# Kernel optimization log

Hardware: AMD Instinct MI355X
Metric: run time of the kernel (lower is better)

## Reference

```python
import jax, jax.numpy as jnp
import numpy as np

N_USERS = 200000
N_ITEMS = 50000
F = 64          # n_factors
B = 32768       # batch of (user, item) pairs
L = 256         # ratings per user (dense-ified ragged lists)
MIN_R = 1
MAX_R = 5


def setup_inputs() -> dict:
    key = jax.random.key(0)
    ks = jax.random.split(key, 8)
    # xavier_normal_ std = sqrt(2 / (fan_in + fan_out))
    std_u = (2.0 / (N_USERS + F)) ** 0.5
    std_i = (2.0 / (N_ITEMS + F)) ** 0.5
    user_factors = jax.random.normal(ks[0], (N_USERS, F), dtype=jnp.float32) * std_u
    item_factors = jax.random.normal(ks[1], (N_ITEMS, F), dtype=jnp.float32) * std_i
    user_biases = jax.random.normal(ks[2], (N_USERS, 1), dtype=jnp.float32)
    item_biases = jax.random.normal(ks[3], (N_ITEMS, 1), dtype=jnp.float32)
    # integer star ratings in [MIN_R, MAX_R], one dense row per user
    ratings = jax.random.randint(ks[4], (N_USERS, L), MIN_R, MAX_R + 1).astype(jnp.float32)
    users = jax.random.randint(ks[5], (B,), 0, N_USERS)
    items = jax.random.randint(ks[6], (B,), 0, N_ITEMS)
    item_pos = jax.random.randint(ks[7], (B,), 0, L)  # position of the item in the user's rating row
    return {
        "users": users, "items": items, "item_pos": item_pos,
        "ratings": ratings,
        "user_factors": user_factors, "item_factors": item_factors,
        "user_biases": user_biases, "item_biases": item_biases,
        "min_rating": MIN_R, "max_rating": MAX_R,
    }


def reference(users, items, item_pos, ratings, user_factors, item_factors,
              user_biases, item_biases, min_rating, max_rating):
    b = users.shape[0]
    # MF prediction: biases + dot(user_factor, item_factor), shape [B, 1]
    pred = (user_biases[users] + item_biases[items]
            + jnp.sum(user_factors[users] * item_factors[items], axis=1, keepdims=True))
    p = pred[:, 0]  # [B]

    # per-sample: user's rating row with this item's rating replaced by the prediction
    rows = ratings[users]                                   # [B, L]
    rows = rows.at[jnp.arange(b), item_pos].set(p)          # batched index-update

    # torch.histc(bins=max_rating, min=min_rating, max=max_rating):
    # width = (max - min) / bins; values outside [min, max] ignored; x == max -> last bin
    bins = max_rating
    width = (max_rating - min_rating) / bins
    idx = jnp.floor((rows - min_rating) / width)
    idx = jnp.where(rows == max_rating, bins - 1, idx)      # [B, L]
    in_range = (rows >= min_rating) & (rows <= max_rating)

    # end bin from rounded prediction: clip(round(p), max(min-1, 0), max-1)
    end = jnp.clip(jnp.round(p), max(min_rating - 1, 0), max_rating - 1)  # [B]

    # mass = sum(hist[0:end+1]) - 0.5 * hist[end]  == count(idx<=end) - 0.5*count(idx==end)
    le = jnp.where(in_range & (idx <= end[:, None]), 1.0, 0.0)
    eq = jnp.where(in_range & (idx == end[:, None]), 1.0, 0.0)
    mass = jnp.sum(le - 0.5 * eq, axis=1, keepdims=True)    # [B, 1]

    return jnp.stack((pred, mass), axis=1)                   # [B, 2, 1]
```

## Files before the change

### kernel.cpp

```cpp
#include <hip/hip_runtime.h>

constexpr int EPW = 8;

__global__ __launch_bounds__(256) void hist_mf_kernel(
    const int*   __restrict__ users,
    const int*   __restrict__ items,
    const int*   __restrict__ item_pos,
    const float* __restrict__ ratings,
    const float* __restrict__ user_factors,
    const float* __restrict__ item_factors,
    const float* __restrict__ user_biases,
    const float* __restrict__ item_biases,
    const int*   __restrict__ minr_p,
    const int*   __restrict__ maxr_p,
    int L, int F, int B,
    float* __restrict__ out)
{
    const int wv   = threadIdx.x >> 6;
    const int lane = threadIdx.x & 63;
    const int wave = blockIdx.x * (blockDim.x >> 6) + wv;
    const int e0   = wave * EPW;
    if (e0 >= B) return;

    const int minr = *minr_p, maxr = *maxr_p;
    const int bins = maxr;
    const float fmin  = (float)minr;
    const float fmax  = (float)maxr;
    const float width = (float)(maxr - minr) / (float)bins;
    const float invw  = 1.0f / width;
    const float lo    = (float)((minr - 1) > 0 ? minr - 1 : 0);
    const float hi    = (float)(maxr - 1);

    int u[EPW], it[EPW], ps[EPW];
    #pragma unroll
    for (int k = 0; k < EPW; ++k) {
        int e = min(e0 + k, B - 1);
        u[k]  = users[e];
        it[k] = items[e];
        ps[k] = item_pos[e];
    }

    const float* rowp[EPW];
    #pragma unroll
    for (int k = 0; k < EPW; ++k) rowp[k] = ratings + (size_t)u[k] * L;

    const int nchunk = ((L & 3) == 0) ? (L >> 8) : 0;
    float4 r4[EPW];
    #pragma unroll
    for (int k = 0; k < EPW; ++k)
        r4[k] = (nchunk > 0) ? reinterpret_cast<const float4*>(rowp[k])[lane]
                             : make_float4(0.f, 0.f, 0.f, 0.f);

    float d[EPW];
    #pragma unroll
    for (int k = 0; k < EPW; ++k) d[k] = 0.f;
    for (int f = lane; f < F; f += 64) {
        #pragma unroll
        for (int k = 0; k < EPW; ++k)
            d[k] += user_factors[(size_t)u[k] * F + f] *
                    item_factors[(size_t)it[k] * F + f];
    }
    #pragma unroll
    for (int o = 32; o > 0; o >>= 1) {
        #pragma unroll
        for (int k = 0; k < EPW; ++k) d[k] += __shfl_xor(d[k], o, 64);
    }

    float pred[EPW], endv[EPW], mass[EPW];
    #pragma unroll
    for (int k = 0; k < EPW; ++k) {
        pred[k] = user_biases[u[k]] + item_biases[it[k]] + d[k];
        endv[k] = fminf(fmaxf(rintf(pred[k]), lo), hi);
        mass[k] = 0.f;
    }

    auto accum = [&](float rraw, int j, int pos, float predv, float ev, float& m) {
        float v = (j == pos) ? predv : rraw;
        bool in = (v >= fmin) && (v <= fmax);
        float fidx = floorf((v - fmin) * invw);
        if (v == fmax) fidx = (float)(bins - 1);
        if (in) {
            if (fidx <= ev) m += 1.0f;
            if (fidx == ev) m -= 0.5f;
        }
    };

    if (nchunk > 0) {
        const int j0 = lane * 4;
        #pragma unroll
        for (int k = 0; k < EPW; ++k) {
            accum(r4[k].x, j0 + 0, ps[k], pred[k], endv[k], mass[k]);
            accum(r4[k].y, j0 + 1, ps[k], pred[k], endv[k], mass[k]);
            accum(r4[k].z, j0 + 2, ps[k], pred[k], endv[k], mass[k]);
            accum(r4[k].w, j0 + 3, ps[k], pred[k], endv[k], mass[k]);
        }
    }
    for (int c = 1; c < nchunk; ++c) {
        const int j0 = c * 256 + lane * 4;
        #pragma unroll
        for (int k = 0; k < EPW; ++k) {
            float4 q = reinterpret_cast<const float4*>(rowp[k] + c * 256)[lane];
            accum(q.x, j0 + 0, ps[k], pred[k], endv[k], mass[k]);
            accum(q.y, j0 + 1, ps[k], pred[k], endv[k], mass[k]);
            accum(q.z, j0 + 2, ps[k], pred[k], endv[k], mass[k]);
            accum(q.w, j0 + 3, ps[k], pred[k], endv[k], mass[k]);
        }
    }
    for (int j = (nchunk << 8) + lane; j < L; j += 64) {
        #pragma unroll
        for (int k = 0; k < EPW; ++k)
            accum(rowp[k][j], j, ps[k], pred[k], endv[k], mass[k]);
    }

    #pragma unroll
    for (int o = 32; o > 0; o >>= 1) {
        #pragma unroll
        for (int k = 0; k < EPW; ++k) mass[k] += __shfl_xor(mass[k], o, 64);
    }

    if (lane == 0) {
        const int nv = min(EPW, B - e0);
        if (nv == EPW) {
            #pragma unroll
            for (int q = 0; q < EPW / 2; ++q)
                reinterpret_cast<float4*>(out)[wave * (EPW / 2) + q] =
                    make_float4(pred[2 * q], mass[2 * q],
                                pred[2 * q + 1], mass[2 * q + 1]);
        } else {
            for (int k = 0; k < nv; ++k) {
                out[2 * (e0 + k) + 0] = pred[k];
                out[2 * (e0 + k) + 1] = mass[k];
            }
        }
    }
}

extern "C" void kernel_launch(void* const* d_in, const int* in_sizes, int n_in,
                              void* d_out, int out_size, void* d_ws, size_t ws_size,
                              hipStream_t stream) {
    const int*   users        = (const int*)  d_in[0];
    const int*   items        = (const int*)  d_in[1];
    const int*   item_pos     = (const int*)  d_in[2];
    const float* ratings      = (const float*)d_in[3];
    const float* user_factors = (const float*)d_in[4];
    const float* item_factors = (const float*)d_in[5];
    const float* user_biases  = (const float*)d_in[6];
    const float* item_biases  = (const float*)d_in[7];
    const int*   minr_p       = (const int*)  d_in[8];
    const int*   maxr_p       = (const int*)  d_in[9];

    const int B       = in_sizes[0];
    const int N_USERS = in_sizes[6];
    const int L       = in_sizes[3] / N_USERS;
    const int F       = in_sizes[4] / N_USERS;

    float* out = (float*)d_out;

    const int elemsPerBlock = (256 / 64) * EPW;
    const int grid = (B + elemsPerBlock - 1) / elemsPerBlock;

    hist_mf_kernel<<<grid, 256, 0, stream>>>(
        users, items, item_pos, ratings, user_factors, item_factors,
        user_biases, item_biases, minr_p, maxr_p, L, F, B, out);
}
```

Baseline: 21.16 us.

## Stage rating rows into LDS via global_load_lds and halve elements per wave

Loads each user's rating row directly from global memory into LDS with the asynchronous global_load_lds builtin, in place of register float4 loads. The kernel then waits on vmcnt and reads the row back from LDS for the histogram step. Elements per wave drop from 8 to 4, which doubles the grid and cuts register pressure, aiming for more memory-level parallelism. The cost is 16KB of LDS per block, which may limit occupancy, plus an extra LDS round trip. The direct-to-LDS path only covers L==256; other lengths use a scalar loop.

```diff
diff --git a/kernel.cpp b/kernel.cpp
--- a/kernel.cpp
+++ b/kernel.cpp
@@ -1,6 +1,10 @@
 #include <hip/hip_runtime.h>
 
-constexpr int EPW = 8;
+constexpr int EPW = 4;
+constexpr int WPB = 4;
+
+typedef const __attribute__((address_space(1))) void GAS;
+typedef __attribute__((address_space(3))) void LAS;
 
 __global__ __launch_bounds__(256) void hist_mf_kernel(
     const int*   __restrict__ users,
@@ -16,9 +20,11 @@
     int L, int F, int B,
     float* __restrict__ out)
 {
+    __shared__ __align__(16) float lds[WPB][EPW][256];
+
     const int wv   = threadIdx.x >> 6;
     const int lane = threadIdx.x & 63;
-    const int wave = blockIdx.x * (blockDim.x >> 6) + wv;
+    const int wave = blockIdx.x * WPB + wv;
     const int e0   = wave * EPW;
     if (e0 >= B) return;
 
@@ -44,12 +50,16 @@
     #pragma unroll
     for (int k = 0; k < EPW; ++k) rowp[k] = ratings + (size_t)u[k] * L;
 
-    const int nchunk = ((L & 3) == 0) ? (L >> 8) : 0;
-    float4 r4[EPW];
-    #pragma unroll
-    for (int k = 0; k < EPW; ++k)
-        r4[k] = (nchunk > 0) ? reinterpret_cast<const float4*>(rowp[k])[lane]
-                             : make_float4(0.f, 0.f, 0.f, 0.f);
+    const bool dma = (L == 256);
+    if (dma) {
+        #pragma unroll
+        for (int k = 0; k < EPW; ++k) {
+            __builtin_amdgcn_global_load_lds(
+                (GAS*)(rowp[k] + lane * 4),
+                (LAS*)&lds[wv][k][lane * 4],
+                16, 0, 0);
+        }
+    }
 
     float d[EPW];
     #pragma unroll
@@ -85,31 +95,24 @@
         }
     };
 
-    if (nchunk > 0) {
+    if (dma) {
+        asm volatile("s_waitcnt vmcnt(0)" ::: "memory");
+        __builtin_amdgcn_sched_barrier(0);
         const int j0 = lane * 4;
         #pragma unroll
         for (int k = 0; k < EPW; ++k) {
-            accum(r4[k].x, j0 + 0, ps[k], pred[k], endv[k], mass[k]);
-            accum(r4[k].y, j0 + 1, ps[k], pred[k], endv[k], mass[k]);
-            accum(r4[k].z, j0 + 2, ps[k], pred[k], endv[k], mass[k]);
-            accum(r4[k].w, j0 + 3, ps[k], pred[k], endv[k], mass[k]);
-        }
-    }
-    for (int c = 1; c < nchunk; ++c) {
-        const int j0 = c * 256 + lane * 4;
-        #pragma unroll
-        for (int k = 0; k < EPW; ++k) {
-            float4 q = reinterpret_cast<const float4*>(rowp[k] + c * 256)[lane];
+            float4 q = *reinterpret_cast<const float4*>(&lds[wv][k][lane * 4]);
             accum(q.x, j0 + 0, ps[k], pred[k], endv[k], mass[k]);
             accum(q.y, j0 + 1, ps[k], pred[k], endv[k], mass[k]);
             accum(q.z, j0 + 2, ps[k], pred[k], endv[k], mass[k]);
             accum(q.w, j0 + 3, ps[k], pred[k], endv[k], mass[k]);
         }
-    }
-    for (int j = (nchunk << 8) + lane; j < L; j += 64) {
-        #pragma unroll
-        for (int k = 0; k < EPW; ++k)
-            accum(rowp[k][j], j, ps[k], pred[k], endv[k], mass[k]);
+    } else {
+        for (int j = lane; j < L; j += 64) {
+            #pragma unroll
+            for (int k = 0; k < EPW; ++k)
+                accum(rowp[k][j], j, ps[k], pred[k], endv[k], mass[k]);
+        }
     }
 
     #pragma unroll
@@ -121,11 +124,10 @@
     if (lane == 0) {
         const int nv = min(EPW, B - e0);
         if (nv == EPW) {
-            #pragma unroll
-            for (int q = 0; q < EPW / 2; ++q)
-                reinterpret_cast<float4*>(out)[wave * (EPW / 2) + q] =
-                    make_float4(pred[2 * q], mass[2 * q],
-                                pred[2 * q + 1], mass[2 * q + 1]);
+            reinterpret_cast<float4*>(out)[2 * wave + 0] =
+                make_float4(pred[0], mass[0], pred[1], mass[1]);
+            reinterpret_cast<float4*>(out)[2 * wave + 1] =
+                make_float4(pred[2], mass[2], pred[3], mass[3]);
         } else {
             for (int k = 0; k < nv; ++k) {
                 out[2 * (e0 + k) + 0] = pred[k];
@@ -156,7 +158,7 @@
 
     float* out = (float*)d_out;
 
-    const int elemsPerBlock = (256 / 64) * EPW;
+    const int elemsPerBlock = WPB * EPW;
     const int grid = (B + elemsPerBlock - 1) / elemsPerBlock;
 
     hist_mf_kernel<<<grid, 256, 0, stream>>>(
```

New measurement: 18.79 us. 1.13x faster.
